# Kernel optimization log

Measured on AMD Instinct MI355X. Metric: run time of the kernel, lower is better.

Reference implementation:

```python
import jax, jax.numpy as jnp
import numpy as np

B, CS, CT, H, W = 16, 512, 512, 64, 64

def setup_inputs() -> dict:
    key = jax.random.key(0)
    k1, k2 = jax.random.split(key)
    x = jax.random.normal(k1, (B, CS, H, W), dtype=jnp.float32)
    # 16 Linear weights, each [out_ch, in_ch] (torch Linear layout), stacked
    Wg = jax.random.normal(k2, (16, CT, CS), dtype=jnp.float32) * (2.0 / CT) ** 0.5
    return {"x": x, "Wg": Wg}

def reference(x, Wg):
    # x: [B, Cs, H, W]; Wg: [16, Ct, Cs] indexed by phase r*4+c, r=(i%4), c=(j%4)
    # Dropout is identity in eval mode (deterministic reference).
    b, cs, h, w = x.shape
    ct = Wg.shape[1]
    Wrq = Wg.reshape(4, 4, ct, cs)               # [r, q, Ct, Cs]
    xr = x.reshape(b, cs, h // 4, 4, w // 4, 4)  # [b, c, h4, r, w4, q]
    # grouped matmul: each (r,q) phase uses its own weight
    out = jnp.einsum('bchrwq,rqoc->bohrwq', xr, Wrq)
    return out.reshape(b, ct, h, w)
```

## Files before the change

kernel.cpp:

```cpp
#include <hip/hip_runtime.h>
#include <stdint.h>


typedef __attribute__((ext_vector_type(8))) short short8;
typedef __attribute__((ext_vector_type(4))) float f32x4;

#define CS 512
#define CT 512
#define HW 4096
#define BK 32
#define MT 128
#define NR 8
#define BPITCH 40
#define BUFB 73728

__device__ __forceinline__ uint16_t f32_to_bf16(float f) {
    uint32_t u = __builtin_bit_cast(uint32_t, f);
    u += 0x7FFFu + ((u >> 16) & 1u);
    return (uint16_t)(u >> 16);
}

__global__ __launch_bounds__(256)
void w2_cvt(const float* __restrict__ Wg, uint16_t* __restrict__ W2) {
    int idx = (blockIdx.x * 256 + threadIdx.x) * 8;
    float4 a = *(const float4*)(Wg + idx);
    float4 b = *(const float4*)(Wg + idx + 4);
    uint16_t o[8];
    o[0]=f32_to_bf16(a.x); o[1]=f32_to_bf16(a.y); o[2]=f32_to_bf16(a.z); o[3]=f32_to_bf16(a.w);
    o[4]=f32_to_bf16(b.x); o[5]=f32_to_bf16(b.y); o[6]=f32_to_bf16(b.z); o[7]=f32_to_bf16(b.w);
    *(short8*)(W2 + idx) = *(short8*)o;
}

template<bool USE_W2>
__global__ __launch_bounds__(512, 2)
void gwl_main(const float* __restrict__ x, const float* __restrict__ Wg,
              const uint16_t* __restrict__ W2, float* __restrict__ out) {
    const int nb = blockIdx.x;
    const int mb = blockIdx.y;
    const int r  = blockIdx.z;
    const int m0 = mb * MT;

    __shared__ __align__(16) unsigned char smem[2 * BUFB];
    float* T = (float*)smem;

    const int tid  = threadIdx.x;
    const int lane = tid & 63;
    const int wave = tid >> 6;
    const int q    = wave & 3;
    const int mw   = wave >> 2;
    const int lr = lane & 15, qd = lane >> 4;

    const int w16 = tid & 15;
    const int rho = (tid >> 4) & 7;
    const int kw  = tid >> 7;
    const int rg  = nb * NR + rho;
    const int bb  = rg >> 4;
    const int h4  = rg & 15;
    const float* bbase = x + (size_t)bb * CS * HW
                           + (size_t)((h4 * 4 + r) * 64 + w16 * 4);

    const uint16_t* abase = USE_W2
        ? W2 + ((size_t)(r * 4 + q) * CT + m0 + mw * 64) * CS : (const uint16_t*)nullptr;

    float4 breg[8];
    auto loadB = [&](int k0) {
        const float* p = bbase + (size_t)(k0 + kw * 8) * HW;
        #pragma unroll
        for (int cc = 0; cc < 8; ++cc) breg[cc] = *(const float4*)(p + (size_t)cc * HW);
    };
    auto writeB = [&](uint16_t* BsD) {
        #pragma unroll
        for (int qq = 0; qq < 4; ++qq) {
            uint16_t tmp[8];
            #pragma unroll
            for (int cc = 0; cc < 8; ++cc)
                tmp[cc] = f32_to_bf16(((const float*)&breg[cc])[qq]);
            *(short8*)(BsD + (qq * 128 + rho * 16 + w16) * BPITCH + kw * 8) = *(short8*)tmp;
        }
    };
    auto stageA_glds = [&](int k0, uint16_t* AsD) {
        #pragma unroll
        for (int t = 0; t < 4; ++t) {
            const uint16_t* src = abase + (size_t)(t * 16 + (lane >> 2)) * CS
                                        + k0 + (((lane & 3) ^ ((lane >> 3) & 3)) * 8);
            uint16_t* dst = AsD + (q * 128 + mw * 64) * 32 + t * 512;
            __builtin_amdgcn_global_load_lds(
                (const __attribute__((address_space(1))) void*)src,
                (__attribute__((address_space(3))) void*)dst, 16, 0, 0);
        }
    };
    auto stageA_fp32 = [&](int k0, uint16_t* AsD) {
        const int qa = tid >> 7, rem = tid & 127;
        const int ka = rem & 7, ma = rem >> 3;
        const float* ap = Wg + ((size_t)(r * 4 + qa) * CT + m0 + ma) * CS + k0 + ka * 4;
        const int kc = (((ka >> 1) ^ ((ma >> 1) & 3)) * 8) + (ka & 1) * 4;
        #pragma unroll
        for (int it = 0; it < 8; ++it) {
            float4 v = *(const float4*)(ap + (size_t)it * 16 * CS);
            uint16_t tmp[4] = {f32_to_bf16(v.x), f32_to_bf16(v.y),
                               f32_to_bf16(v.z), f32_to_bf16(v.w)};
            *(uint64_t*)(AsD + (qa * 128 + ma + it * 16) * 32 + kc) =
                *(const uint64_t*)tmp;
        }
    };

    f32x4 acc[4][8] = {};

    {
        uint16_t* As0 = (uint16_t*)smem;
        uint16_t* Bs0 = (uint16_t*)(smem + 32768);
        loadB(0);
        if (USE_W2) stageA_glds(0, As0); else stageA_fp32(0, As0);
        writeB(Bs0);
        loadB(BK);
        __syncthreads();
    }

    for (int k = 0; k < 16; ++k) {
        const uint16_t* Asq = (const uint16_t*)(smem + (k & 1) * BUFB)
                              + (q * 128 + mw * 64) * 32;
        const uint16_t* Bsq = (const uint16_t*)(smem + (k & 1) * BUFB + 32768)
                              + q * 128 * BPITCH;
        short8 afr[4], bfr[8];
        #pragma unroll
        for (int i = 0; i < 4; ++i)
            afr[i] = *(const short8*)(Asq + (i * 16 + lr) * 32
                                      + ((qd ^ ((lr >> 1) & 3)) * 8));
        #pragma unroll
        for (int j = 0; j < 8; ++j)
            bfr[j] = *(const short8*)(Bsq + (j * 16 + lr) * BPITCH + qd * 8);

        if (k < 15) {
            uint16_t* AsN = (uint16_t*)(smem + ((k + 1) & 1) * BUFB);
            uint16_t* BsN = (uint16_t*)(smem + ((k + 1) & 1) * BUFB + 32768);
            if (USE_W2) stageA_glds((k + 1) * BK, AsN); else stageA_fp32((k + 1) * BK, AsN);
            __builtin_amdgcn_sched_barrier(0x38F);
            writeB(BsN);
            if (k < 14) loadB((k + 2) * BK);
        }

        #pragma unroll
        for (int i = 0; i < 4; ++i)
            #pragma unroll
            for (int j = 0; j < 8; ++j)
                acc[i][j] = __builtin_amdgcn_mfma_f32_16x16x32_bf16(
                    afr[i], bfr[j], acc[i][j], 0, 0, 0);

        if (k < 15) {
            if (k < 14) asm volatile("s_waitcnt vmcnt(8)" ::: "memory");
            else        asm volatile("s_waitcnt vmcnt(0)" ::: "memory");
            asm volatile("s_waitcnt lgkmcnt(0)" ::: "memory");
            __builtin_amdgcn_s_barrier();
        }
    }

    const int m16s = tid >> 5;
    const int rs   = (tid >> 2) & 7;
    const int ws   = (tid & 3) * 16;
    const int rgs  = nb * NR + rs;
    const int obb  = rgs >> 4;
    const int oh4  = rgs & 15;
    #pragma unroll
    for (int ic = 0; ic < 8; ++ic) {
        __syncthreads();
        if (mw == (ic >> 2)) {
            const int i = ic & 3;
            #pragma unroll
            for (int j = 0; j < 8; ++j)
                #pragma unroll
                for (int g = 0; g < 4; ++g)
                    T[((qd * 4 + g) * 8 + j) * 68 + lr * 4 + q] = acc[i][j][g];
        }
        __syncthreads();
        float* op = out + ((size_t)obb * CT + m0 + ic * 16 + m16s) * HW
                        + (oh4 * 4 + r) * 64 + ws;
        const float* tp = T + (m16s * 8 + rs) * 68 + ws;
        #pragma unroll
        for (int c = 0; c < 4; ++c)
            ((float4*)op)[c] = ((const float4*)tp)[c];
    }
}

extern "C" void kernel_launch(void* const* d_in, const int* in_sizes, int n_in,
                              void* d_out, int out_size, void* d_ws, size_t ws_size,
                              hipStream_t stream) {
    const float* x  = (const float*)d_in[0];
    const float* Wg = (const float*)d_in[1];
    float* out = (float*)d_out;
    dim3 grid(32, 4, 4);
    if (ws_size >= (size_t)16 * 512 * 512 * 2) {
        uint16_t* W2 = (uint16_t*)d_ws;
        w2_cvt<<<2048, 256, 0, stream>>>(Wg, W2);
        gwl_main<true><<<grid, 512, 0, stream>>>(x, Wg, W2, out);
    } else {
        gwl_main<false><<<grid, 512, 0, stream>>>(x, Wg, nullptr, out);
    }
}
```

Baseline: 298.4 us.

## Pre-transpose activations to bf16 and stage both operands via direct global-to-LDS loads

Adds a pre-pass kernel that converts x to bf16 and lays it out per phase, channel-contiguous, in workspace. With that layout the main GEMM can stage both the A and B tiles with global_load_lds instead of converting fp32 B in registers. The main loop is also reorganised to issue the stage two steps ahead after a barrier, and MFMA priority is raised with s_setprio. In exchange it adds an extra pass that reads all of x and writes a 64 MB bf16 copy, plus a larger workspace requirement, and the old fp32 path is kept as a separate fallback kernel.

```diff
diff --git a/kernel.cpp b/kernel.cpp
--- a/kernel.cpp
+++ b/kernel.cpp
@@ -11,8 +11,9 @@
 #define BK 32
 #define MT 128
 #define NR 8
-#define BPITCH 40
-#define BUFB 73728
+#define ABYTES 32768
+#define BBYTES 32768
+#define BUFB (ABYTES + BBYTES)
 
 __device__ __forceinline__ uint16_t f32_to_bf16(float f) {
     uint32_t u = __builtin_bit_cast(uint32_t, f);
@@ -31,10 +32,41 @@
     *(short8*)(W2 + idx) = *(short8*)o;
 }
 
-template<bool USE_W2>
+__global__ __launch_bounds__(256)
+void xt_cvt(const float* __restrict__ x, uint16_t* __restrict__ xT) {
+    const int c0 = blockIdx.x * 64;
+    const int h  = blockIdx.y;
+    const int b  = blockIdx.z;
+    const int r = h & 3, h4 = h >> 2, rg = b * 16 + h4;
+    __shared__ float L[64][65];
+    const int tid = threadIdx.x;
+    const int wr = tid & 15;
+    const int cr = tid >> 4;
+    const float* src = x + (((size_t)b * CS + c0 + cr) * 64 + h) * 64 + wr * 4;
+    #pragma unroll
+    for (int it = 0; it < 4; ++it) {
+        float4 v = *(const float4*)(src + (size_t)it * 16 * HW);
+        L[cr + it * 16][wr * 4 + 0] = v.x;
+        L[cr + it * 16][wr * 4 + 1] = v.y;
+        L[cr + it * 16][wr * 4 + 2] = v.z;
+        L[cr + it * 16][wr * 4 + 3] = v.w;
+    }
+    __syncthreads();
+    const int orow = tid >> 2;
+    const int q = orow >> 4, w16 = orow & 15;
+    const int cc = (tid & 3) * 16;
+    const int w = w16 * 4 + q;
+    uint16_t tmp[16];
+    #pragma unroll
+    for (int i = 0; i < 16; ++i) tmp[i] = f32_to_bf16(L[cc + i][w]);
+    uint16_t* dst = xT + ((((size_t)(r * 4 + q) * 256 + rg) * 16 + w16) * 512 + c0 + cc);
+    *(short8*)(dst)     = *(short8*)(tmp);
+    *(short8*)(dst + 8) = *(short8*)(tmp + 8);
+}
+
 __global__ __launch_bounds__(512, 2)
-void gwl_main(const float* __restrict__ x, const float* __restrict__ Wg,
-              const uint16_t* __restrict__ W2, float* __restrict__ out) {
+void gwl_main(const uint16_t* __restrict__ W2, const uint16_t* __restrict__ xT,
+              float* __restrict__ out) {
     const int nb = blockIdx.x;
     const int mb = blockIdx.y;
     const int r  = blockIdx.z;
@@ -50,106 +82,69 @@
     const int mw   = wave >> 2;
     const int lr = lane & 15, qd = lane >> 4;
 
-    const int w16 = tid & 15;
-    const int rho = (tid >> 4) & 7;
-    const int kw  = tid >> 7;
-    const int rg  = nb * NR + rho;
-    const int bb  = rg >> 4;
-    const int h4  = rg & 15;
-    const float* bbase = x + (size_t)bb * CS * HW
-                           + (size_t)((h4 * 4 + r) * 64 + w16 * 4);
-
-    const uint16_t* abase = USE_W2
-        ? W2 + ((size_t)(r * 4 + q) * CT + m0 + mw * 64) * CS : (const uint16_t*)nullptr;
-
-    float4 breg[8];
-    auto loadB = [&](int k0) {
-        const float* p = bbase + (size_t)(k0 + kw * 8) * HW;
-        #pragma unroll
-        for (int cc = 0; cc < 8; ++cc) breg[cc] = *(const float4*)(p + (size_t)cc * HW);
+    const int lrow = lane >> 2;
+    const int swz  = ((lane & 3) ^ ((lane >> 3) & 3)) * 8;
+
+    const uint16_t* abase = W2 + ((size_t)(r * 4 + q) * CT + m0 + mw * 64) * CS;
+    const uint16_t* bbase = xT + (((size_t)(r * 4 + q) * 256 + nb * 8 + mw * 4) * 16) * 512;
+
+    auto stage = [&](int k0, int bufn) {
+        uint16_t* As = (uint16_t*)(smem + bufn * BUFB) + (q * 128 + mw * 64) * 32;
+        uint16_t* Bs = (uint16_t*)(smem + bufn * BUFB + ABYTES) + (q * 128 + mw * 64) * 32;
+        #pragma unroll
+        for (int t = 0; t < 4; ++t) {
+            const uint16_t* asrc = abase + (size_t)(t * 16 + lrow) * CS + k0 + swz;
+            __builtin_amdgcn_global_load_lds(
+                (const __attribute__((address_space(1))) void*)asrc,
+                (__attribute__((address_space(3))) void*)(As + t * 512), 16, 0, 0);
+        }
+        #pragma unroll
+        for (int t = 0; t < 4; ++t) {
+            const uint16_t* bsrc = bbase + ((size_t)t * 16 + lrow) * 512 + k0 + swz;
+            __builtin_amdgcn_global_load_lds(
+                (const __attribute__((address_space(1))) void*)bsrc,
+                (__attribute__((address_space(3))) void*)(Bs + t * 512), 16, 0, 0);
+        }
     };
-    auto writeB = [&](uint16_t* BsD) {
-        #pragma unroll
-        for (int qq = 0; qq < 4; ++qq) {
-            uint16_t tmp[8];
-            #pragma unroll
-            for (int cc = 0; cc < 8; ++cc)
-                tmp[cc] = f32_to_bf16(((const float*)&breg[cc])[qq]);
-            *(short8*)(BsD + (qq * 128 + rho * 16 + w16) * BPITCH + kw * 8) = *(short8*)tmp;
-        }
-    };
-    auto stageA_glds = [&](int k0, uint16_t* AsD) {
-        #pragma unroll
-        for (int t = 0; t < 4; ++t) {
-            const uint16_t* src = abase + (size_t)(t * 16 + (lane >> 2)) * CS
-                                        + k0 + (((lane & 3) ^ ((lane >> 3) & 3)) * 8);
-            uint16_t* dst = AsD + (q * 128 + mw * 64) * 32 + t * 512;
-            __builtin_amdgcn_global_load_lds(
-                (const __attribute__((address_space(1))) void*)src,
-                (__attribute__((address_space(3))) void*)dst, 16, 0, 0);
-        }
-    };
-    auto stageA_fp32 = [&](int k0, uint16_t* AsD) {
-        const int qa = tid >> 7, rem = tid & 127;
-        const int ka = rem & 7, ma = rem >> 3;
-        const float* ap = Wg + ((size_t)(r * 4 + qa) * CT + m0 + ma) * CS + k0 + ka * 4;
-        const int kc = (((ka >> 1) ^ ((ma >> 1) & 3)) * 8) + (ka & 1) * 4;
-        #pragma unroll
-        for (int it = 0; it < 8; ++it) {
-            float4 v = *(const float4*)(ap + (size_t)it * 16 * CS);
-            uint16_t tmp[4] = {f32_to_bf16(v.x), f32_to_bf16(v.y),
-                               f32_to_bf16(v.z), f32_to_bf16(v.w)};
-            *(uint64_t*)(AsD + (qa * 128 + ma + it * 16) * 32 + kc) =
-                *(const uint64_t*)tmp;
-        }
-    };
 
     f32x4 acc[4][8] = {};
 
-    {
-        uint16_t* As0 = (uint16_t*)smem;
-        uint16_t* Bs0 = (uint16_t*)(smem + 32768);
-        loadB(0);
-        if (USE_W2) stageA_glds(0, As0); else stageA_fp32(0, As0);
-        writeB(Bs0);
-        loadB(BK);
-        __syncthreads();
-    }
-
+    stage(0, 0);
+    stage(BK, 1);
+    asm volatile("s_waitcnt vmcnt(8)" ::: "memory");
+    __builtin_amdgcn_s_barrier();
+
+    const int rdswz = (qd ^ ((lr >> 1) & 3)) * 8;
     for (int k = 0; k < 16; ++k) {
-        const uint16_t* Asq = (const uint16_t*)(smem + (k & 1) * BUFB)
+        const int buf = k & 1;
+        const uint16_t* Asq = (const uint16_t*)(smem + buf * BUFB)
                               + (q * 128 + mw * 64) * 32;
-        const uint16_t* Bsq = (const uint16_t*)(smem + (k & 1) * BUFB + 32768)
-                              + q * 128 * BPITCH;
+        const uint16_t* Bsq = (const uint16_t*)(smem + buf * BUFB + ABYTES)
+                              + q * 128 * 32;
         short8 afr[4], bfr[8];
         #pragma unroll
         for (int i = 0; i < 4; ++i)
-            afr[i] = *(const short8*)(Asq + (i * 16 + lr) * 32
-                                      + ((qd ^ ((lr >> 1) & 3)) * 8));
+            afr[i] = *(const short8*)(Asq + (i * 16 + lr) * 32 + rdswz);
         #pragma unroll
         for (int j = 0; j < 8; ++j)
-            bfr[j] = *(const short8*)(Bsq + (j * 16 + lr) * BPITCH + qd * 8);
-
-        if (k < 15) {
-            uint16_t* AsN = (uint16_t*)(smem + ((k + 1) & 1) * BUFB);
-            uint16_t* BsN = (uint16_t*)(smem + ((k + 1) & 1) * BUFB + 32768);
-            if (USE_W2) stageA_glds((k + 1) * BK, AsN); else stageA_fp32((k + 1) * BK, AsN);
-            __builtin_amdgcn_sched_barrier(0x38F);
-            writeB(BsN);
-            if (k < 14) loadB((k + 2) * BK);
-        }
-
+            bfr[j] = *(const short8*)(Bsq + (j * 16 + lr) * 32 + rdswz);
+        asm volatile("s_waitcnt lgkmcnt(0)" ::: "memory");
+        __builtin_amdgcn_sched_barrier(0);
+        __builtin_amdgcn_s_barrier();
+        if (k < 14) stage((k + 2) * BK, buf);
+
+        __builtin_amdgcn_s_setprio(1);
         #pragma unroll
         for (int i = 0; i < 4; ++i)
             #pragma unroll
             for (int j = 0; j < 8; ++j)
                 acc[i][j] = __builtin_amdgcn_mfma_f32_16x16x32_bf16(
                     afr[i], bfr[j], acc[i][j], 0, 0, 0);
+        __builtin_amdgcn_s_setprio(0);
 
         if (k < 15) {
             if (k < 14) asm volatile("s_waitcnt vmcnt(8)" ::: "memory");
             else        asm volatile("s_waitcnt vmcnt(0)" ::: "memory");
-            asm volatile("s_waitcnt lgkmcnt(0)" ::: "memory");
             __builtin_amdgcn_s_barrier();
         }
     }
@@ -181,6 +176,118 @@
     }
 }
 
+#define BPITCH 40
+#define FBUFB 73728
+
+__global__ __launch_bounds__(512, 2)
+void gwl_fb(const float* __restrict__ x, const float* __restrict__ Wg,
+            float* __restrict__ out) {
+    const int nb = blockIdx.x, mb = blockIdx.y, r = blockIdx.z;
+    const int m0 = mb * MT;
+    __shared__ __align__(16) unsigned char smem[2 * FBUFB];
+    float* T = (float*)smem;
+    const int tid = threadIdx.x, lane = tid & 63, wave = tid >> 6;
+    const int q = wave & 3, mw = wave >> 2;
+    const int lr = lane & 15, qd = lane >> 4;
+    const int w16 = tid & 15, rho = (tid >> 4) & 7, kw = tid >> 7;
+    const int rg = nb * NR + rho, bb = rg >> 4, h4 = rg & 15;
+    const float* bbase = x + (size_t)bb * CS * HW
+                           + (size_t)((h4 * 4 + r) * 64 + w16 * 4);
+    float4 breg[8];
+    auto loadB = [&](int k0) {
+        const float* p = bbase + (size_t)(k0 + kw * 8) * HW;
+        #pragma unroll
+        for (int cc = 0; cc < 8; ++cc) breg[cc] = *(const float4*)(p + (size_t)cc * HW);
+    };
+    auto writeB = [&](uint16_t* BsD) {
+        #pragma unroll
+        for (int qq = 0; qq < 4; ++qq) {
+            uint16_t tmp[8];
+            #pragma unroll
+            for (int cc = 0; cc < 8; ++cc)
+                tmp[cc] = f32_to_bf16(((const float*)&breg[cc])[qq]);
+            *(short8*)(BsD + (qq * 128 + rho * 16 + w16) * BPITCH + kw * 8) = *(short8*)tmp;
+        }
+    };
+    auto stageA = [&](int k0, uint16_t* AsD) {
+        const int qa = tid >> 7, rem = tid & 127;
+        const int ka = rem & 7, ma = rem >> 3;
+        const float* ap = Wg + ((size_t)(r * 4 + qa) * CT + m0 + ma) * CS + k0 + ka * 4;
+        const int kc = (((ka >> 1) ^ ((ma >> 1) & 3)) * 8) + (ka & 1) * 4;
+        #pragma unroll
+        for (int it = 0; it < 8; ++it) {
+            float4 v = *(const float4*)(ap + (size_t)it * 16 * CS);
+            uint16_t tmp[4] = {f32_to_bf16(v.x), f32_to_bf16(v.y),
+                               f32_to_bf16(v.z), f32_to_bf16(v.w)};
+            *(uint64_t*)(AsD + (qa * 128 + ma + it * 16) * 32 + kc) =
+                *(const uint64_t*)tmp;
+        }
+    };
+    f32x4 acc[4][8] = {};
+    {
+        uint16_t* As0 = (uint16_t*)smem;
+        uint16_t* Bs0 = (uint16_t*)(smem + 32768);
+        loadB(0);
+        stageA(0, As0);
+        writeB(Bs0);
+        loadB(BK);
+        __syncthreads();
+    }
+    for (int k = 0; k < 16; ++k) {
+        const uint16_t* Asq = (const uint16_t*)(smem + (k & 1) * FBUFB)
+                              + (q * 128 + mw * 64) * 32;
+        const uint16_t* Bsq = (const uint16_t*)(smem + (k & 1) * FBUFB + 32768)
+                              + q * 128 * BPITCH;
+        short8 afr[4], bfr[8];
+        #pragma unroll
+        for (int i = 0; i < 4; ++i)
+            afr[i] = *(const short8*)(Asq + (i * 16 + lr) * 32
+                                      + ((qd ^ ((lr >> 1) & 3)) * 8));
+        #pragma unroll
+        for (int j = 0; j < 8; ++j)
+            bfr[j] = *(const short8*)(Bsq + (j * 16 + lr) * BPITCH + qd * 8);
+        if (k < 15) {
+            uint16_t* AsN = (uint16_t*)(smem + ((k + 1) & 1) * FBUFB);
+            uint16_t* BsN = (uint16_t*)(smem + ((k + 1) & 1) * FBUFB + 32768);
+            stageA((k + 1) * BK, AsN);
+            writeB(BsN);
+            if (k < 14) loadB((k + 2) * BK);
+        }
+        #pragma unroll
+        for (int i = 0; i < 4; ++i)
+            #pragma unroll
+            for (int j = 0; j < 8; ++j)
+                acc[i][j] = __builtin_amdgcn_mfma_f32_16x16x32_bf16(
+                    afr[i], bfr[j], acc[i][j], 0, 0, 0);
+        if (k < 15) {
+            asm volatile("s_waitcnt vmcnt(0)" ::: "memory");
+            asm volatile("s_waitcnt lgkmcnt(0)" ::: "memory");
+            __builtin_amdgcn_s_barrier();
+        }
+    }
+    const int m16s = tid >> 5, rs = (tid >> 2) & 7, ws = (tid & 3) * 16;
+    const int rgs = nb * NR + rs, obb = rgs >> 4, oh4 = rgs & 15;
+    #pragma unroll
+    for (int ic = 0; ic < 8; ++ic) {
+        __syncthreads();
+        if (mw == (ic >> 2)) {
+            const int i = ic & 3;
+            #pragma unroll
+            for (int j = 0; j < 8; ++j)
+                #pragma unroll
+                for (int g = 0; g < 4; ++g)
+                    T[((qd * 4 + g) * 8 + j) * 68 + lr * 4 + q] = acc[i][j][g];
+        }
+        __syncthreads();
+        float* op = out + ((size_t)obb * CT + m0 + ic * 16 + m16s) * HW
+                        + (oh4 * 4 + r) * 64 + ws;
+        const float* tp = T + (m16s * 8 + rs) * 68 + ws;
+        #pragma unroll
+        for (int c = 0; c < 4; ++c)
+            ((float4*)op)[c] = ((const float4*)tp)[c];
+    }
+}
+
 extern "C" void kernel_launch(void* const* d_in, const int* in_sizes, int n_in,
                               void* d_out, int out_size, void* d_ws, size_t ws_size,
                               hipStream_t stream) {
@@ -188,11 +295,15 @@
     const float* Wg = (const float*)d_in[1];
     float* out = (float*)d_out;
     dim3 grid(32, 4, 4);
-    if (ws_size >= (size_t)16 * 512 * 512 * 2) {
+    const size_t w2_elems = (size_t)16 * 512 * 512;
+    const size_t xt_elems = (size_t)4 * 4 * 256 * 16 * 512;
+    if (ws_size >= (w2_elems + xt_elems) * 2) {
         uint16_t* W2 = (uint16_t*)d_ws;
+        uint16_t* xT = (uint16_t*)d_ws + w2_elems;
         w2_cvt<<<2048, 256, 0, stream>>>(Wg, W2);
-        gwl_main<true><<<grid, 512, 0, stream>>>(x, Wg, W2, out);
+        xt_cvt<<<dim3(8, 64, 16), 256, 0, stream>>>(x, xT);
+        gwl_main<<<grid, 512, 0, stream>>>(W2, xT, out);
     } else {
-        gwl_main<false><<<grid, 512, 0, stream>>>(x, Wg, nullptr, out);
-    }
-}
+        gwl_fb<<<grid, 512, 0, stream>>>(x, Wg, out);
+    }
+}
```

New measurement: 323.2 us. 8.3% more time.
